# Kernel optimization log

Measured on AMD Instinct MI355X. Metric: run time of the kernel, lower is better.

## Reference

```python
import jax, jax.numpy as jnp
import numpy as np

N_GRAPHS = 32
NODES = 4096          # nodes per graph
D_IN = 128
HID = 16
OUT_DIM = 39
N = N_GRAPHS * NODES  # 131072 total nodes
E = N * 32            # avg degree 32 -> 4194304 edges


def setup_inputs() -> dict:
    key = jax.random.key(0)
    ks = jax.random.split(key, 7)
    x = jax.random.normal(ks[0], (N, D_IN), dtype=jnp.float32)
    # edges constrained within each graph (PyG Batch semantics)
    src_local = jax.random.randint(ks[1], (E,), 0, NODES)
    dst_local = jax.random.randint(ks[2], (E,), 0, NODES)
    graph_of_edge = jnp.arange(E, dtype=jnp.int64) % N_GRAPHS
    offset = graph_of_edge * NODES
    edge_index = jnp.stack([src_local.astype(jnp.int64) + offset,
                            dst_local.astype(jnp.int64) + offset], axis=0)
    W_l = jax.random.normal(ks[3], (HID, D_IN), dtype=jnp.float32) * 0.05
    b_l = jnp.zeros((HID,), dtype=jnp.float32)
    W_r = jax.random.normal(ks[4], (HID, D_IN), dtype=jnp.float32) * 0.05
    W_out = jax.random.normal(ks[5], (OUT_DIM, NODES * HID), dtype=jnp.float32) * 0.01
    b_out = jnp.zeros((OUT_DIM,), dtype=jnp.float32)
    return {"x": x, "edge_index": edge_index, "W_l": W_l, "b_l": b_l,
            "W_r": W_r, "W_out": W_out, "b_out": b_out}


def reference(x, edge_index, W_l, b_l, W_r, W_out, b_out):
    src, dst = edge_index[0], edge_index[1]
    # SAGEConv (mean aggr): lin_l(mean_{j in N(i)} x_j) + lin_r(x_i)
    # Linear commutes with mean: transform first (D_IN -> HID) to shrink gather traffic.
    xl = x @ W_l.T                                      # [N, HID]
    agg = jax.ops.segment_sum(xl[src], dst, num_segments=N)   # [N, HID]
    cnt = jax.ops.segment_sum(jnp.ones((E,), x.dtype), dst, num_segments=N)
    mean = agg / jnp.maximum(cnt, 1.0)[:, None]         # zero-degree nodes -> 0
    h = jax.nn.relu(mean + b_l + x @ W_r.T)             # [N, HID]
    # per-graph flatten + shared Linear (the Python loop in torch == batched matmul)
    g = h.reshape(N_GRAPHS, NODES * HID)                # [G, NODES*HID]
    out = g @ W_out.T + b_out                           # [G, OUT_DIM]
    return out[:, :, None]                              # [G, OUT_DIM, 1] (unsqueeze(1) per-graph, stacked)
```

## Files before the change

### kernel.cpp

```cpp
#include <hip/hip_runtime.h>

#define NG 32
#define NODES 4096
#define NTOT (NG * NODES)
#define DIN 128
#define HID 16
#define ODIM 39
#define NEDGE (NTOT * 32)

typedef unsigned int uint;
typedef unsigned short ushort;

#define NB   8192
#define BCAP 768
#define KHB  256
#define EPB  (NEDGE / KHB)

#define WS_XL     0
#define WS_XR     2097152
#define WS_AGG    4194304
#define WS_CNT    6291456
#define WS_GCOUNT 6422528
#define PEDGE_BYTE_OFF ((size_t)(6422528 + 8192) * 4)
#define WS_NEED_FAST (PEDGE_BYTE_OFF + (size_t)NB * BCAP * 2)

__device__ __forceinline__ int scan_perm(int r) { return ((r & 31) << 3) | (r >> 5); }

__global__ __launch_bounds__(256) void k1_lin(const float* __restrict__ x,
                                              const float* __restrict__ Wl,
                                              const float* __restrict__ Wr,
                                              float* __restrict__ xl,
                                              float* __restrict__ xr) {
    __shared__ float xs[64 * 132];
    __shared__ float wls[16 * 132];
    __shared__ float wrs[16 * 132];
    const int t = threadIdx.x;

    #pragma unroll
    for (int i = 0; i < 2; ++i) {
        int f = i * 256 + t;
        int o = f >> 5, k4 = f & 31;
        float4 a = reinterpret_cast<const float4*>(Wl)[f];
        float4 b = reinterpret_cast<const float4*>(Wr)[f];
        *reinterpret_cast<float4*>(&wls[o * 132 + 4 * k4]) = a;
        *reinterpret_cast<float4*>(&wrs[o * 132 + 4 * k4]) = b;
    }

    const long base = (long)blockIdx.x * 64;
    const float4* xg = reinterpret_cast<const float4*>(x) + base * 32;
    #pragma unroll
    for (int i = 0; i < 8; ++i) {
        int f = i * 256 + t;
        int n = f >> 5, k4 = f & 31;
        *reinterpret_cast<float4*>(&xs[n * 132 + 4 * k4]) = xg[f];
    }
    __syncthreads();

    const int o = t & 15, ngrp = t >> 4;
    float accl[4] = {0.f, 0.f, 0.f, 0.f};
    float accr[4] = {0.f, 0.f, 0.f, 0.f};
    for (int k4 = 0; k4 < 32; ++k4) {
        float4 w0 = *reinterpret_cast<const float4*>(&wls[o * 132 + 4 * k4]);
        float4 w1 = *reinterpret_cast<const float4*>(&wrs[o * 132 + 4 * k4]);
        #pragma unroll
        for (int j = 0; j < 4; ++j) {
            float4 xv = *reinterpret_cast<const float4*>(&xs[(ngrp + 16 * j) * 132 + 4 * k4]);
            accl[j] += xv.x * w0.x + xv.y * w0.y + xv.z * w0.z + xv.w * w0.w;
            accr[j] += xv.x * w1.x + xv.y * w1.y + xv.z * w1.z + xv.w * w1.w;
        }
    }
    #pragma unroll
    for (int j = 0; j < 4; ++j) {
        long n = base + ngrp + 16 * j;
        xl[n * HID + o] = accl[j];
        xr[n * HID + o] = accr[j];
    }
}

__global__ __launch_bounds__(1024) void kH_hist(const int* __restrict__ ei,
                                                uint* __restrict__ hist_t) {
    __shared__ uint lh[NB];
    const int t = threadIdx.x;
    const int blk = blockIdx.x;
    for (int i = t; i < NB; i += 1024) lh[i] = 0u;
    __syncthreads();
    const int e0 = blk * EPB;
    #pragma unroll
    for (int j = 0; j < EPB / 1024; ++j) {
        int e = e0 + j * 1024 + t;
        uint dl = (uint)ei[NEDGE + e] & 4095u;
        uint b = (uint)(t & 31) * 256u + (dl >> 4);
        atomicAdd(&lh[b], 1u);
    }
    __syncthreads();
    for (int i = t; i < NB; i += 1024) hist_t[(size_t)blk * NB + i] = lh[i];
}

__global__ __launch_bounds__(256) void kScan32(uint* __restrict__ hist_t,
                                               uint* __restrict__ gcount) {
    __shared__ uint tile[256 * 33];
    __shared__ uint part[32 * 9];
    const int B = blockIdx.x, t = threadIdx.x;
    const int b0 = B * 32;
    const int cb = t & 31;
    const int rb = t >> 5;

    #pragma unroll
    for (int ch = 0; ch < 32; ++ch) {
        int r = ch * 8 + rb;
        tile[r * 33 + cb] = hist_t[(size_t)scan_perm(r) * NB + b0 + cb];
    }
    __syncthreads();

    const int g2 = t >> 3, l = t & 7;
    {
        uint s = 0u;
        #pragma unroll
        for (int k = 0; k < 32; ++k) s += tile[(l * 32 + k) * 33 + g2];
        part[g2 * 9 + l] = s;
    }
    __syncthreads();
    uint excl = 0u;
    #pragma unroll
    for (int l2 = 0; l2 < 8; ++l2) {
        uint pv = part[g2 * 9 + l2];
        if (l2 < l) excl += pv;
        if (l == 7 && l2 == 7) gcount[b0 + g2] = excl + pv;
    }
    {
        uint run = excl;
        #pragma unroll
        for (int k = 0; k < 32; ++k) {
            uint tmp = tile[(l * 32 + k) * 33 + g2];
            tile[(l * 32 + k) * 33 + g2] = run;
            run += tmp;
        }
    }
    __syncthreads();

    #pragma unroll
    for (int ch = 0; ch < 32; ++ch) {
        int r = ch * 8 + rb;
        hist_t[(size_t)scan_perm(r) * NB + b0 + cb] = tile[r * 33 + cb];
    }
}

__global__ __launch_bounds__(1024) void kB2_place(const int* __restrict__ ei,
                                                  const uint* __restrict__ hist_t,
                                                  ushort* __restrict__ pedge) {
    __shared__ uint lp[NB];
    const int t = threadIdx.x;
    const int blk = blockIdx.x;
    for (int i = t; i < NB; i += 1024) lp[i] = hist_t[(size_t)blk * NB + i];
    __syncthreads();
    const int e0 = blk * EPB;
    #pragma unroll
    for (int j = 0; j < EPB / 1024; ++j) {
        int e = e0 + j * 1024 + t;
        uint sl = (uint)ei[e] & 4095u;
        uint dl = (uint)ei[NEDGE + e] & 4095u;
        uint b = (uint)(t & 31) * 256u + (dl >> 4);
        uint pos = atomicAdd(&lp[b], 1u);
        if (pos < BCAP)
            pedge[(size_t)b * BCAP + pos] = (ushort)(sl | ((dl & 15u) << 12));
    }
}

__global__ __launch_bounds__(256) void kS_reg(const uint* __restrict__ gcount,
                                              const ushort* __restrict__ pedge,
                                              const float* __restrict__ xl,
                                              float* __restrict__ agg,
                                              float* __restrict__ cnt) {
    __shared__ ushort eb[BCAP];
    __shared__ ushort sorted[BCAP];
    __shared__ uint c16[16];
    __shared__ uint off16[16];
    __shared__ uint cur16[16];
    const int b = blockIdx.x;
    const int g = b >> 8, seg = b & 255;
    const int t = threadIdx.x;

    if (t < 16) c16[t] = 0u;
    int n = (int)gcount[b];
    if (n > BCAP) n = BCAP;
    const size_t bo = (size_t)b * BCAP;
    for (int i = t; i < n; i += 256) eb[i] = pedge[bo + i];
    __syncthreads();

    for (int i = t; i < n; i += 256) atomicAdd(&c16[eb[i] >> 12], 1u);
    __syncthreads();

    if (t == 0) {
        uint run = 0u;
        #pragma unroll
        for (int d = 0; d < 16; ++d) {
            off16[d] = run;
            cur16[d] = run;
            run += c16[d];
        }
    }
    __syncthreads();

    for (int i = t; i < n; i += 256) {
        ushort p = eb[i];
        uint pos = atomicAdd(&cur16[p >> 12], 1u);
        sorted[pos] = (ushort)(p & 4095u);
    }
    __syncthreads();

    const int dlo = t >> 4, c = t & 15;
    const uint start = off16[dlo];
    const uint len = c16[dlo];
    const float* xrow = xl + (((size_t)g << 12) * HID) + c;
    float acc = 0.f;
    for (uint i = 0; i < len; ++i) {
        int sl = sorted[start + i];
        acc += xrow[(size_t)sl * HID];
    }

    agg[(((size_t)g << 12) + (seg << 4)) * HID + t] = acc;
    if (t < 16) cnt[((size_t)g << 12) + (seg << 4) + t] = (float)c16[t];
}

__global__ __launch_bounds__(256) void k2_edges(const int* __restrict__ ei,
                                                const float* __restrict__ xl,
                                                float* __restrict__ agg,
                                                float* __restrict__ cnt) {
    const long tid = (long)blockIdx.x * 256 + threadIdx.x;
    const int e = (int)(tid >> 4);
    const int c = (int)(tid & 15);
    const int s = ei[e];
    const int d = ei[NEDGE + e];
    const float v = xl[(long)s * HID + c];
    atomicAdd(&agg[(long)d * HID + c], v);
    if (c == 0) atomicAdd(&cnt[d], 1.0f);
}

__global__ __launch_bounds__(256) void k3_init_out(const float* __restrict__ bout,
                                                   float* __restrict__ out) {
    int i = blockIdx.x * 256 + threadIdx.x;
    if (i < NG * ODIM) out[i] = bout[i % ODIM];
}

__global__ __launch_bounds__(256) void k4_out(const float* __restrict__ agg,
                                              const float* __restrict__ cnt,
                                              const float* __restrict__ xr,
                                              const float* __restrict__ bl,
                                              const float* __restrict__ Wout,
                                              float* __restrict__ out) {
    __shared__ float hs[32 * 128];
    __shared__ float wt[39 * 132];
    const int t = threadIdx.x;
    const int kbase = blockIdx.x * 128;

    #pragma unroll
    for (int r = 0; r < 16; ++r) {
        int idx = r * 256 + t;
        int g = idx >> 7, kk = idx & 127;
        long flat = (long)g * (NODES * HID) + kbase + kk;
        float a = agg[flat];
        float xv = xr[flat];
        float cn = cnt[(g << 12) + ((kbase + kk) >> 4)];
        float h = a / fmaxf(cn, 1.0f) + bl[kk & 15] + xv;
        hs[g * 128 + kk] = fmaxf(h, 0.0f);
    }
    for (int idx = t; idx < ODIM * 128; idx += 256) {
        int od = idx >> 7, kk = idx & 127;
        wt[od * 132 + kk] = Wout[(long)od * (NODES * HID) + kbase + kk];
    }
    __syncthreads();

    const int tod = t & 31, tg = t >> 5;
    const int od0 = tod;
    const bool has1 = (tod + 32) < ODIM;
    const int od1 = has1 ? tod + 32 : tod;
    float acc0[4] = {0.f, 0.f, 0.f, 0.f};
    float acc1[4] = {0.f, 0.f, 0.f, 0.f};
    for (int k4 = 0; k4 < 32; ++k4) {
        float4 w0 = *reinterpret_cast<const float4*>(&wt[od0 * 132 + 4 * k4]);
        float4 w1 = *reinterpret_cast<const float4*>(&wt[od1 * 132 + 4 * k4]);
        #pragma unroll
        for (int j = 0; j < 4; ++j) {
            float4 h4 = *reinterpret_cast<const float4*>(&hs[(tg * 4 + j) * 128 + 4 * k4]);
            acc0[j] += h4.x * w0.x + h4.y * w0.y + h4.z * w0.z + h4.w * w0.w;
            acc1[j] += h4.x * w1.x + h4.y * w1.y + h4.z * w1.z + h4.w * w1.w;
        }
    }
    #pragma unroll
    for (int j = 0; j < 4; ++j) {
        int g = tg * 4 + j;
        atomicAdd(&out[g * ODIM + od0], acc0[j]);
        if (has1) atomicAdd(&out[g * ODIM + od1], acc1[j]);
    }
}

extern "C" void kernel_launch(void* const* d_in, const int* in_sizes, int n_in,
                              void* d_out, int out_size, void* d_ws, size_t ws_size,
                              hipStream_t stream) {
    const float* x    = (const float*)d_in[0];
    const int*   ei   = (const int*)d_in[1];
    const float* Wl   = (const float*)d_in[2];
    const float* bl   = (const float*)d_in[3];
    const float* Wr   = (const float*)d_in[4];
    const float* Wout = (const float*)d_in[5];
    const float* bout = (const float*)d_in[6];
    float* out = (float*)d_out;
    float* ws  = (float*)d_ws;

    float* xl  = ws + WS_XL;
    float* xr  = ws + WS_XR;
    float* agg = ws + WS_AGG;
    float* cnt = ws + WS_CNT;

    if (ws_size >= WS_NEED_FAST) {
        uint*   hist_t = (uint*)(ws + WS_AGG);
        uint*   gcount = (uint*)(ws + WS_GCOUNT);
        ushort* pedge  = (ushort*)((char*)d_ws + PEDGE_BYTE_OFF);

        k1_lin<<<NTOT / 64, 256, 0, stream>>>(x, Wl, Wr, xl, xr);
        kH_hist<<<KHB, 1024, 0, stream>>>(ei, hist_t);
        kScan32<<<NB / 32, 256, 0, stream>>>(hist_t, gcount);
        kB2_place<<<KHB, 1024, 0, stream>>>(ei, hist_t, pedge);
        kS_reg<<<NB, 256, 0, stream>>>(gcount, pedge, xl, agg, cnt);
        k3_init_out<<<(NG * ODIM + 255) / 256, 256, 0, stream>>>(bout, out);
        k4_out<<<(NODES * HID) / 128, 256, 0, stream>>>(agg, cnt, xr, bl, Wout, out);
    } else {
        hipMemsetAsync(agg, 0, (size_t)(NTOT * HID + NTOT) * sizeof(float), stream);
        k1_lin<<<NTOT / 64, 256, 0, stream>>>(x, Wl, Wr, xl, xr);
        k2_edges<<<(long)NEDGE * 16 / 256, 256, 0, stream>>>(ei, xl, agg, cnt);
        k3_init_out<<<(NG * ODIM + 255) / 256, 256, 0, stream>>>(bout, out);
        k4_out<<<(NODES * HID) / 128, 256, 0, stream>>>(agg, cnt, xr, bl, Wout, out);
    }
}
```

Measured before the change: 141.6 us.

## Replace atomic output GEMV with split-K partial tiles and a separate reduction kernel

Replaces the init-plus-atomic output stage with a split-K kernel. Each of 1024 blocks computes h for a 64-wide K slice across all 32 graphs, stages W_out and h in shared memory, and writes a 32x39 partial tile to workspace. A second kernel reduces the partials and adds the bias. This drops the output-init launch and the atomics on the output, but writes and rereads about 5 MB of partials and reuses the pedge workspace region for them.

```diff
diff --git a/kernel.cpp b/kernel.cpp
--- a/kernel.cpp
+++ b/kernel.cpp
@@ -15,6 +15,9 @@
 #define BCAP 768
 #define KHB  256
 #define EPB  (NEDGE / KHB)
+
+#define K4B  1024
+#define PODS 40
 
 #define WS_XL     0
 #define WS_XR     2097152
@@ -222,6 +225,83 @@
     if (t < 16) cnt[((size_t)g << 12) + (seg << 4) + t] = (float)c16[t];
 }
 
+__global__ __launch_bounds__(256) void k4b_out(const float* __restrict__ agg,
+                                               const float* __restrict__ cnt,
+                                               const float* __restrict__ xr,
+                                               const float* __restrict__ bl,
+                                               const float* __restrict__ Wout,
+                                               float* __restrict__ partial) {
+    __shared__ float hs[32 * 64];
+    __shared__ float wt[39 * 68];
+    const int t = threadIdx.x;
+    const int kb = blockIdx.x;
+    const int kbase = kb * 64;
+
+    #pragma unroll
+    for (int r = 0; r < 8; ++r) {
+        int idx = r * 256 + t;
+        int g = idx >> 6, kk = idx & 63;
+        long flat = (long)g * (NODES * HID) + kbase + kk;
+        float a = agg[flat];
+        float xv = xr[flat];
+        float cn = cnt[(g << 12) + ((kbase + kk) >> 4)];
+        float h = a / fmaxf(cn, 1.0f) + bl[kk & 15] + xv;
+        hs[g * 64 + kk] = fmaxf(h, 0.0f);
+    }
+    for (int idx = t; idx < ODIM * 64; idx += 256) {
+        int od = idx >> 6, kk = idx & 63;
+        wt[od * 68 + kk] = Wout[(long)od * (NODES * HID) + kbase + kk];
+    }
+    __syncthreads();
+
+    const int tod = t & 31, tg = t >> 5;
+    const int od0 = tod;
+    const bool has1 = (tod + 32) < ODIM;
+    const int od1 = has1 ? tod + 32 : tod;
+    float acc0[4] = {0.f, 0.f, 0.f, 0.f};
+    float acc1[4] = {0.f, 0.f, 0.f, 0.f};
+    for (int k4 = 0; k4 < 16; ++k4) {
+        float4 w0 = *reinterpret_cast<const float4*>(&wt[od0 * 68 + 4 * k4]);
+        float4 w1 = *reinterpret_cast<const float4*>(&wt[od1 * 68 + 4 * k4]);
+        #pragma unroll
+        for (int j = 0; j < 4; ++j) {
+            float4 h4 = *reinterpret_cast<const float4*>(&hs[(tg * 4 + j) * 64 + 4 * k4]);
+            acc0[j] += h4.x * w0.x + h4.y * w0.y + h4.z * w0.z + h4.w * w0.w;
+            acc1[j] += h4.x * w1.x + h4.y * w1.y + h4.z * w1.z + h4.w * w1.w;
+        }
+    }
+    float* pb = partial + (size_t)kb * (NG * PODS);
+    #pragma unroll
+    for (int j = 0; j < 4; ++j) {
+        int g = tg * 4 + j;
+        pb[g * PODS + od0] = acc0[j];
+        if (has1) pb[g * PODS + od1] = acc1[j];
+    }
+}
+
+__global__ __launch_bounds__(256) void kR_reduce(const float* __restrict__ partial,
+                                                 const float* __restrict__ bout,
+                                                 float* __restrict__ out) {
+    __shared__ float red[6 * PODS];
+    const int g = blockIdx.x, t = threadIdx.x;
+    if (t < 240) {
+        const int grp = t / PODS, od = t % PODS;
+        float acc = 0.f;
+        if (od < ODIM) {
+            for (int kb = grp; kb < K4B; kb += 6)
+                acc += partial[(size_t)kb * (NG * PODS) + g * PODS + od];
+        }
+        red[grp * PODS + od] = acc;
+    }
+    __syncthreads();
+    if (t < ODIM) {
+        float s = bout[t];
+        #pragma unroll
+        for (int grp = 0; grp < 6; ++grp) s += red[grp * PODS + t];
+        out[g * ODIM + t] = s;
+    }
+}
+
 __global__ __launch_bounds__(256) void k2_edges(const int* __restrict__ ei,
                                                 const float* __restrict__ xl,
                                                 float* __restrict__ agg,
@@ -313,17 +393,18 @@
     float* cnt = ws + WS_CNT;
 
     if (ws_size >= WS_NEED_FAST) {
-        uint*   hist_t = (uint*)(ws + WS_AGG);
-        uint*   gcount = (uint*)(ws + WS_GCOUNT);
-        ushort* pedge  = (ushort*)((char*)d_ws + PEDGE_BYTE_OFF);
+        uint*   hist_t  = (uint*)(ws + WS_AGG);
+        uint*   gcount  = (uint*)(ws + WS_GCOUNT);
+        ushort* pedge   = (ushort*)((char*)d_ws + PEDGE_BYTE_OFF);
+        float*  partial = (float*)((char*)d_ws + PEDGE_BYTE_OFF);
 
         k1_lin<<<NTOT / 64, 256, 0, stream>>>(x, Wl, Wr, xl, xr);
         kH_hist<<<KHB, 1024, 0, stream>>>(ei, hist_t);
         kScan32<<<NB / 32, 256, 0, stream>>>(hist_t, gcount);
         kB2_place<<<KHB, 1024, 0, stream>>>(ei, hist_t, pedge);
         kS_reg<<<NB, 256, 0, stream>>>(gcount, pedge, xl, agg, cnt);
-        k3_init_out<<<(NG * ODIM + 255) / 256, 256, 0, stream>>>(bout, out);
-        k4_out<<<(NODES * HID) / 128, 256, 0, stream>>>(agg, cnt, xr, bl, Wout, out);
+        k4b_out<<<K4B, 256, 0, stream>>>(agg, cnt, xr, bl, Wout, partial);
+        kR_reduce<<<NG, 256, 0, stream>>>(partial, bout, out);
     } else {
         hipMemsetAsync(agg, 0, (size_t)(NTOT * HID + NTOT) * sizeof(float), stream);
         k1_lin<<<NTOT / 64, 256, 0, stream>>>(x, Wl, Wr, xl, xr);
```

New measurement: 182.9 us. 1.29x slower.
